# Optimization experiments

Measured on AMD Instinct MI355X. Metric: run time of the kernel, lower is better.

The kernel has to match this reference:

```python
import jax, jax.numpy as jnp
import numpy as np
from jax import lax


def setup_inputs() -> dict:
    key = jax.random.key(0)
    k1, k2 = jax.random.split(key)
    B, N, C, H, W = 4, 32, 32, 64, 64
    x = jax.random.normal(k1, (B, N, C, H, W), dtype=jnp.float32)
    # grouped conv weight: groups = N*C, 1 input channel per group, 3 outputs per group
    w = jax.random.normal(k2, (3 * N * C, 1, 1, 1), dtype=jnp.float32) * 0.1
    return {"x": x, "w": w}


def reference(x, w):
    B, N, C, H, W = x.shape
    xc = x.reshape(B, N * C, H, W)
    # grouped 1x1 conv (groups = N*C), matches nn.Conv2d(inC*N, 3*qkvC*N, 1, groups=qkvC*N, bias=False)
    qkv = lax.conv_general_dilated(
        xc, w,
        window_strides=(1, 1), padding=[(0, 0), (0, 0)],
        feature_group_count=N * C,
        dimension_numbers=("NCHW", "OIHW", "NCHW"),
    )
    qkv = qkv.reshape(B, N, C, 3, H, W)
    scale = (H * W) ** (-0.5)
    q = scale * qkv[:, :, :, 0]           # (B,N,C,H,W)
    k = qkv[:, :, :, 1]
    v = qkv[:, :, :, 2]
    # original: 6D einsum (a,b,c,d,e,f) then sum over d,e == contraction over H,W
    S = jnp.einsum("bachw,bfchw->bcaf", q, k)   # (B,C,N,N)
    A = jax.nn.softmax(S, axis=-1)
    # original: broadcast-multiply with v and sum over f
    out = jnp.einsum("bcaf,bfchw->abchw", A, v)  # (N,B,C,H,W)
    return out
```

## Files before the change

### kernel.cpp

```cpp
#include <hip/hip_runtime.h>

typedef __attribute__((ext_vector_type(8))) short bf16x8;
typedef __attribute__((ext_vector_type(4))) float f32x4;

#define BB 4
#define NN 32
#define CC 32
#define HWD 4096
#define AROW ((size_t)CC * HWD)

__device__ __forceinline__ unsigned cvt_pk_bf16(float lo, float hi) {
    unsigned r;
    asm("v_cvt_pk_bf16_f32 %0, %1, %2" : "=v"(r) : "v"(lo), "v"(hi));
    return r;
}

__device__ __forceinline__ bf16x8 pack8(float4 a, float4 b) {
    union { unsigned u[4]; bf16x8 v; } u;
    u.u[0] = cvt_pk_bf16(a.x, a.y);
    u.u[1] = cvt_pk_bf16(a.z, a.w);
    u.u[2] = cvt_pk_bf16(b.x, b.y);
    u.u[3] = cvt_pk_bf16(b.z, b.w);
    return u.v;
}

__global__ __launch_bounds__(256) void k_gram(const float* __restrict__ x,
                                              float* __restrict__ Gp) {
    const int bid = blockIdx.x;
    const int s   = bid & 7;
    const int bc  = bid >> 3;
    const int b   = bc >> 5, c = bc & 31;
    const int tid = threadIdx.x;
    const int w   = tid >> 6, l = tid & 63;
    const int r   = l & 15, g = l >> 4;

    const float* xb = x + ((size_t)b * NN * CC + c) * HWD;
    const int hwbase = s * 512 + w * 128;
    const float* p0 = xb + (size_t)r        * AROW + hwbase + 8 * g;
    const float* p1 = xb + (size_t)(r + 16) * AROW + hwbase + 8 * g;

    f32x4 acc[2][2];
#pragma unroll
    for (int i = 0; i < 2; ++i)
#pragma unroll
        for (int j = 0; j < 2; ++j)
#pragma unroll
            for (int q = 0; q < 4; ++q) acc[i][j][q] = 0.f;

#pragma unroll
    for (int ch = 0; ch < 4; ++ch) {
        const float4 a0 = *(const float4*)(p0 + ch * 32);
        const float4 a1 = *(const float4*)(p0 + ch * 32 + 4);
        const float4 b0 = *(const float4*)(p1 + ch * 32);
        const float4 b1 = *(const float4*)(p1 + ch * 32 + 4);
        const bf16x8 F0 = pack8(a0, a1);
        const bf16x8 F1 = pack8(b0, b1);
        acc[0][0] = __builtin_amdgcn_mfma_f32_16x16x32_bf16(F0, F0, acc[0][0], 0, 0, 0);
        acc[0][1] = __builtin_amdgcn_mfma_f32_16x16x32_bf16(F0, F1, acc[0][1], 0, 0, 0);
        acc[1][0] = __builtin_amdgcn_mfma_f32_16x16x32_bf16(F1, F0, acc[1][0], 0, 0, 0);
        acc[1][1] = __builtin_amdgcn_mfma_f32_16x16x32_bf16(F1, F1, acc[1][1], 0, 0, 0);
    }

    __shared__ float red[4][64][16];
#pragma unroll
    for (int ta = 0; ta < 2; ++ta)
#pragma unroll
        for (int tf = 0; tf < 2; ++tf)
#pragma unroll
            for (int q = 0; q < 4; ++q)
                red[w][l][(ta * 2 + tf) * 4 + q] = acc[ta][tf][q];
    __syncthreads();

    const int a   = tid >> 3;
    const int f0  = 4 * (tid & 7);
    const int lg  = ((a >> 2) & 3) * 16 + (f0 & 15);
    const int reg = ((a >> 4) * 2 + (f0 >> 4)) * 4 + (a & 3);
    float sv[4];
#pragma unroll
    for (int j = 0; j < 4; ++j) {
        float v = 0.f;
#pragma unroll
        for (int ww = 0; ww < 4; ++ww) v += red[ww][lg + j][reg];
        sv[j] = v;
    }
    *(float4*)&Gp[(size_t)bid * 1024 + 4 * tid] = make_float4(sv[0], sv[1], sv[2], sv[3]);
}

__global__ __launch_bounds__(256) void k_pv(const float* __restrict__ x,
                                            const float* __restrict__ w,
                                            const float* __restrict__ Gp,
                                            float* __restrict__ out) {
    const int bid   = blockIdx.x;
    const int chunk = bid & 15;
    const int bc    = bid >> 4;
    const int b     = bc >> 5, c = bc & 31;
    const int tid   = threadIdx.x;
    const int wv    = tid >> 6, l = tid & 63;
    const int r     = l & 15, g = l >> 4;

    __shared__ unsigned xt[256][16];
    __shared__ unsigned ahat[32][20];

    {
        const int a = tid >> 3, fo = 4 * (tid & 7);
        float gs[4] = {0.f, 0.f, 0.f, 0.f};
#pragma unroll
        for (int s = 0; s < 8; ++s) {
            const float4 v = *(const float4*)&Gp[(size_t)(bc * 8 + s) * 1024 + a * 32 + fo];
            gs[0] += v.x; gs[1] += v.y; gs[2] += v.z; gs[3] += v.w;
        }
        const float wq = w[(a * CC + c) * 3] * 0.015625f;
        float S[4];
#pragma unroll
        for (int j = 0; j < 4; ++j)
            S[j] = wq * w[((fo + j) * CC + c) * 3 + 1] * gs[j];

        float m = fmaxf(fmaxf(S[0], S[1]), fmaxf(S[2], S[3]));
#pragma unroll
        for (int o = 1; o < 8; o <<= 1) m = fmaxf(m, __shfl_xor(m, o, 64));
        float e[4], sum = 0.f;
#pragma unroll
        for (int j = 0; j < 4; ++j) { e[j] = __expf(S[j] - m); sum += e[j]; }
#pragma unroll
        for (int o = 1; o < 8; o <<= 1) sum += __shfl_xor(sum, o, 64);
        const float inv = 1.f / sum;

        const float o0 = e[0] * inv * w[((fo + 0) * CC + c) * 3 + 2];
        const float o1 = e[1] * inv * w[((fo + 1) * CC + c) * 3 + 2];
        const float o2 = e[2] * inv * w[((fo + 2) * CC + c) * 3 + 2];
        const float o3 = e[3] * inv * w[((fo + 3) * CC + c) * 3 + 2];
        ahat[a][2 * (tid & 7) + 0] = cvt_pk_bf16(o0, o1);
        ahat[a][2 * (tid & 7) + 1] = cvt_pk_bf16(o2, o3);
    }

    {
        const int p = tid >> 4;
        const int q = tid & 15;
        const float* xr0 = x + ((size_t)(b * NN + 2 * p) * CC + c) * HWD + chunk * 256;
        const float* xr1 = xr0 + AROW;
#pragma unroll
        for (int k = 0; k < 4; ++k) {
            const int hwc = 4 * (q + 16 * k);
            const float4 fa = *(const float4*)(xr0 + hwc);
            const float4 fb = *(const float4*)(xr1 + hwc);
            const float av[4] = {fa.x, fa.y, fa.z, fa.w};
            const float bv[4] = {fb.x, fb.y, fb.z, fb.w};
#pragma unroll
            for (int i = 0; i < 4; ++i) {
                const int hw = hwc + i;
                xt[hw][p ^ (hw & 12)] = cvt_pk_bf16(av[i], bv[i]);
            }
        }
    }
    __syncthreads();

    const bf16x8 A0 = *(const bf16x8*)&ahat[r][4 * g];
    const bf16x8 A1 = *(const bf16x8*)&ahat[r + 16][4 * g];
    const f32x4 zero = {0.f, 0.f, 0.f, 0.f};

#pragma unroll
    for (int ht = 0; ht < 4; ++ht) {
        const int hw = wv * 64 + ht * 16 + r;
        const bf16x8 B = *(const bf16x8*)&xt[hw][4 * (g ^ ((hw >> 2) & 3))];
        f32x4 d0 = __builtin_amdgcn_mfma_f32_16x16x32_bf16(A0, B, zero, 0, 0, 0);
        f32x4 d1 = __builtin_amdgcn_mfma_f32_16x16x32_bf16(A1, B, zero, 0, 0, 0);

        const size_t hwg = (size_t)chunk * 256 + hw;
#pragma unroll
        for (int q2 = 0; q2 < 4; ++q2) {
            const int a0r = g * 4 + q2;
            out[(((size_t)a0r * BB + b) * CC + c) * HWD + hwg]        = d0[q2];
            out[(((size_t)(a0r + 16) * BB + b) * CC + c) * HWD + hwg] = d1[q2];
        }
    }
}

extern "C" void kernel_launch(void* const* d_in, const int* in_sizes, int n_in,
                              void* d_out, int out_size, void* d_ws, size_t ws_size,
                              hipStream_t stream) {
    const float* x = (const float*)d_in[0];
    const float* w = (const float*)d_in[1];
    float* outp = (float*)d_out;
    float* Gp = (float*)d_ws;

    hipLaunchKernelGGL(k_gram, dim3(1024), dim3(256), 0, stream, x, Gp);
    hipLaunchKernelGGL(k_pv,   dim3(2048), dim3(256), 0, stream, x, w, Gp, outp);
}
```

Before: 45.81 us.

## Fuse gram and PV kernels into one launch with last-block softmax and flag spin-wait

Merges the two kernels into a single 1024-block kernel. Each block computes its partial Gram slice, and the last block per (b,c), found via an atomic counter, reduces the slices, applies the softmax and writes the bf16 A-hat to global memory. It then releases a flag that the other blocks spin on before each does two PV chunks. This removes one kernel launch and the serialization gap between them, and lets blocks reuse x while it is likely still cached. In exchange it adds a memset, spin-waits that rely on all blocks of a group being co-resident, and atomic-load overhead.

```diff
diff --git a/kernel.cpp b/kernel.cpp
--- a/kernel.cpp
+++ b/kernel.cpp
@@ -8,6 +8,10 @@
 #define CC 32
 #define HWD 4096
 #define AROW ((size_t)CC * HWD)
+
+#define GP_BYTES   ((size_t)4 * 1024 * 1024)
+#define AHAT_BYTES ((size_t)256 * 1024)
+#define CTRL_OFF   (GP_BYTES + AHAT_BYTES)
 
 __device__ __forceinline__ unsigned cvt_pk_bf16(float lo, float hi) {
     unsigned r;
@@ -24,90 +28,97 @@
     return u.v;
 }
 
-__global__ __launch_bounds__(256) void k_gram(const float* __restrict__ x,
-                                              float* __restrict__ Gp) {
+__global__ __launch_bounds__(256, 4) void k_all(const float* __restrict__ x,
+                                                const float* __restrict__ w,
+                                                float* __restrict__ Gp,
+                                                unsigned* __restrict__ Ahat,
+                                                unsigned* __restrict__ cnt,
+                                                unsigned* __restrict__ flag,
+                                                float* __restrict__ out) {
     const int bid = blockIdx.x;
     const int s   = bid & 7;
     const int bc  = bid >> 3;
     const int b   = bc >> 5, c = bc & 31;
     const int tid = threadIdx.x;
-    const int w   = tid >> 6, l = tid & 63;
+    const int wv  = tid >> 6, l = tid & 63;
     const int r   = l & 15, g = l >> 4;
 
-    const float* xb = x + ((size_t)b * NN * CC + c) * HWD;
-    const int hwbase = s * 512 + w * 128;
-    const float* p0 = xb + (size_t)r        * AROW + hwbase + 8 * g;
-    const float* p1 = xb + (size_t)(r + 16) * AROW + hwbase + 8 * g;
-
-    f32x4 acc[2][2];
-#pragma unroll
-    for (int i = 0; i < 2; ++i)
-#pragma unroll
-        for (int j = 0; j < 2; ++j)
-#pragma unroll
-            for (int q = 0; q < 4; ++q) acc[i][j][q] = 0.f;
-
-#pragma unroll
-    for (int ch = 0; ch < 4; ++ch) {
-        const float4 a0 = *(const float4*)(p0 + ch * 32);
-        const float4 a1 = *(const float4*)(p0 + ch * 32 + 4);
-        const float4 b0 = *(const float4*)(p1 + ch * 32);
-        const float4 b1 = *(const float4*)(p1 + ch * 32 + 4);
-        const bf16x8 F0 = pack8(a0, a1);
-        const bf16x8 F1 = pack8(b0, b1);
-        acc[0][0] = __builtin_amdgcn_mfma_f32_16x16x32_bf16(F0, F0, acc[0][0], 0, 0, 0);
-        acc[0][1] = __builtin_amdgcn_mfma_f32_16x16x32_bf16(F0, F1, acc[0][1], 0, 0, 0);
-        acc[1][0] = __builtin_amdgcn_mfma_f32_16x16x32_bf16(F1, F0, acc[1][0], 0, 0, 0);
-        acc[1][1] = __builtin_amdgcn_mfma_f32_16x16x32_bf16(F1, F1, acc[1][1], 0, 0, 0);
-    }
-
-    __shared__ float red[4][64][16];
-#pragma unroll
-    for (int ta = 0; ta < 2; ++ta)
-#pragma unroll
-        for (int tf = 0; tf < 2; ++tf)
-#pragma unroll
-            for (int q = 0; q < 4; ++q)
-                red[w][l][(ta * 2 + tf) * 4 + q] = acc[ta][tf][q];
+    __shared__ union {
+        float red[4][64][16];
+        unsigned xt[256][16];
+    } sm;
+    __shared__ unsigned is_last;
+
+    {
+        const float* xb = x + ((size_t)b * NN * CC + c) * HWD;
+        const int hwbase = s * 512 + wv * 128;
+        const float* p0 = xb + (size_t)r        * AROW + hwbase + 8 * g;
+        const float* p1 = xb + (size_t)(r + 16) * AROW + hwbase + 8 * g;
+
+        f32x4 acc[2][2];
+#pragma unroll
+        for (int i = 0; i < 2; ++i)
+#pragma unroll
+            for (int j = 0; j < 2; ++j)
+#pragma unroll
+                for (int q = 0; q < 4; ++q) acc[i][j][q] = 0.f;
+
+#pragma unroll
+        for (int ch = 0; ch < 4; ++ch) {
+            const float4 a0 = *(const float4*)(p0 + ch * 32);
+            const float4 a1 = *(const float4*)(p0 + ch * 32 + 4);
+            const float4 b0 = *(const float4*)(p1 + ch * 32);
+            const float4 b1 = *(const float4*)(p1 + ch * 32 + 4);
+            const bf16x8 F0 = pack8(a0, a1);
+            const bf16x8 F1 = pack8(b0, b1);
+            acc[0][0] = __builtin_amdgcn_mfma_f32_16x16x32_bf16(F0, F0, acc[0][0], 0, 0, 0);
+            acc[0][1] = __builtin_amdgcn_mfma_f32_16x16x32_bf16(F0, F1, acc[0][1], 0, 0, 0);
+            acc[1][0] = __builtin_amdgcn_mfma_f32_16x16x32_bf16(F1, F0, acc[1][0], 0, 0, 0);
+            acc[1][1] = __builtin_amdgcn_mfma_f32_16x16x32_bf16(F1, F1, acc[1][1], 0, 0, 0);
+        }
+
+#pragma unroll
+        for (int ta = 0; ta < 2; ++ta)
+#pragma unroll
+            for (int tf = 0; tf < 2; ++tf)
+#pragma unroll
+                for (int q = 0; q < 4; ++q)
+                    sm.red[wv][l][(ta * 2 + tf) * 4 + q] = acc[ta][tf][q];
+        __syncthreads();
+
+        const int a   = tid >> 3;
+        const int f0  = 4 * (tid & 7);
+        const int lg  = ((a >> 2) & 3) * 16 + (f0 & 15);
+        const int reg = ((a >> 4) * 2 + (f0 >> 4)) * 4 + (a & 3);
+        float sv[4];
+#pragma unroll
+        for (int j = 0; j < 4; ++j) {
+            float v = 0.f;
+#pragma unroll
+            for (int ww = 0; ww < 4; ++ww) v += sm.red[ww][lg + j][reg];
+            sv[j] = v;
+        }
+        *(float4*)&Gp[(size_t)bid * 1024 + 4 * tid] = make_float4(sv[0], sv[1], sv[2], sv[3]);
+    }
+
     __syncthreads();
-
-    const int a   = tid >> 3;
-    const int f0  = 4 * (tid & 7);
-    const int lg  = ((a >> 2) & 3) * 16 + (f0 & 15);
-    const int reg = ((a >> 4) * 2 + (f0 >> 4)) * 4 + (a & 3);
-    float sv[4];
-#pragma unroll
-    for (int j = 0; j < 4; ++j) {
-        float v = 0.f;
-#pragma unroll
-        for (int ww = 0; ww < 4; ++ww) v += red[ww][lg + j][reg];
-        sv[j] = v;
-    }
-    *(float4*)&Gp[(size_t)bid * 1024 + 4 * tid] = make_float4(sv[0], sv[1], sv[2], sv[3]);
-}
-
-__global__ __launch_bounds__(256) void k_pv(const float* __restrict__ x,
-                                            const float* __restrict__ w,
-                                            const float* __restrict__ Gp,
-                                            float* __restrict__ out) {
-    const int bid   = blockIdx.x;
-    const int chunk = bid & 15;
-    const int bc    = bid >> 4;
-    const int b     = bc >> 5, c = bc & 31;
-    const int tid   = threadIdx.x;
-    const int wv    = tid >> 6, l = tid & 63;
-    const int r     = l & 15, g = l >> 4;
-
-    __shared__ unsigned xt[256][16];
-    __shared__ unsigned ahat[32][20];
-
-    {
+    if (tid == 0) {
+        __threadfence();
+        unsigned old = atomicAdd(&cnt[bc], 1u);
+        is_last = (old == 7u) ? 1u : 0u;
+    }
+    __syncthreads();
+
+    if (is_last) {
         const int a = tid >> 3, fo = 4 * (tid & 7);
         float gs[4] = {0.f, 0.f, 0.f, 0.f};
 #pragma unroll
-        for (int s = 0; s < 8; ++s) {
-            const float4 v = *(const float4*)&Gp[(size_t)(bc * 8 + s) * 1024 + a * 32 + fo];
-            gs[0] += v.x; gs[1] += v.y; gs[2] += v.z; gs[3] += v.w;
+        for (int s2 = 0; s2 < 8; ++s2) {
+            const float* gp = &Gp[(size_t)(bc * 8 + s2) * 1024 + a * 32 + fo];
+            gs[0] += __hip_atomic_load(gp + 0, __ATOMIC_RELAXED, __HIP_MEMORY_SCOPE_AGENT);
+            gs[1] += __hip_atomic_load(gp + 1, __ATOMIC_RELAXED, __HIP_MEMORY_SCOPE_AGENT);
+            gs[2] += __hip_atomic_load(gp + 2, __ATOMIC_RELAXED, __HIP_MEMORY_SCOPE_AGENT);
+            gs[3] += __hip_atomic_load(gp + 3, __ATOMIC_RELAXED, __HIP_MEMORY_SCOPE_AGENT);
         }
         const float wq = w[(a * CC + c) * 3] * 0.015625f;
         float S[4];
@@ -129,48 +140,75 @@
         const float o1 = e[1] * inv * w[((fo + 1) * CC + c) * 3 + 2];
         const float o2 = e[2] * inv * w[((fo + 2) * CC + c) * 3 + 2];
         const float o3 = e[3] * inv * w[((fo + 3) * CC + c) * 3 + 2];
-        ahat[a][2 * (tid & 7) + 0] = cvt_pk_bf16(o0, o1);
-        ahat[a][2 * (tid & 7) + 1] = cvt_pk_bf16(o2, o3);
-    }
-
+        unsigned* ad = Ahat + (size_t)bc * 512 + a * 16 + 2 * (tid & 7);
+        __hip_atomic_store(ad + 0, cvt_pk_bf16(o0, o1), __ATOMIC_RELAXED, __HIP_MEMORY_SCOPE_AGENT);
+        __hip_atomic_store(ad + 1, cvt_pk_bf16(o2, o3), __ATOMIC_RELAXED, __HIP_MEMORY_SCOPE_AGENT);
+        __syncthreads();
+        if (tid == 0) {
+            __threadfence();
+            __hip_atomic_store(&flag[bc], 1u, __ATOMIC_RELEASE, __HIP_MEMORY_SCOPE_AGENT);
+        }
+    }
+
+    if (tid == 0) {
+        while (__hip_atomic_load(&flag[bc], __ATOMIC_ACQUIRE, __HIP_MEMORY_SCOPE_AGENT) == 0u)
+            __builtin_amdgcn_s_sleep(2);
+    }
+    __syncthreads();
+
+    union { unsigned u[4]; bf16x8 v; } ua0, ua1;
     {
-        const int p = tid >> 4;
-        const int q = tid & 15;
-        const float* xr0 = x + ((size_t)(b * NN + 2 * p) * CC + c) * HWD + chunk * 256;
-        const float* xr1 = xr0 + AROW;
-#pragma unroll
-        for (int k = 0; k < 4; ++k) {
-            const int hwc = 4 * (q + 16 * k);
-            const float4 fa = *(const float4*)(xr0 + hwc);
-            const float4 fb = *(const float4*)(xr1 + hwc);
-            const float av[4] = {fa.x, fa.y, fa.z, fa.w};
-            const float bv[4] = {fb.x, fb.y, fb.z, fb.w};
-#pragma unroll
-            for (int i = 0; i < 4; ++i) {
-                const int hw = hwc + i;
-                xt[hw][p ^ (hw & 12)] = cvt_pk_bf16(av[i], bv[i]);
+        const unsigned* ad = Ahat + (size_t)bc * 512;
+#pragma unroll
+        for (int i = 0; i < 4; ++i) {
+            ua0.u[i] = __hip_atomic_load(ad + r * 16 + 4 * g + i,
+                                         __ATOMIC_RELAXED, __HIP_MEMORY_SCOPE_AGENT);
+            ua1.u[i] = __hip_atomic_load(ad + (r + 16) * 16 + 4 * g + i,
+                                         __ATOMIC_RELAXED, __HIP_MEMORY_SCOPE_AGENT);
+        }
+    }
+
+    const f32x4 zero = {0.f, 0.f, 0.f, 0.f};
+#pragma clang loop unroll(disable)
+    for (int ck = 0; ck < 2; ++ck) {
+        const int chunk = 2 * s + ck;
+        __syncthreads();
+
+        {
+            const int p = tid >> 4;
+            const int q = tid & 15;
+            const float* xr0 = x + ((size_t)(b * NN + 2 * p) * CC + c) * HWD + chunk * 256;
+            const float* xr1 = xr0 + AROW;
+#pragma unroll
+            for (int k = 0; k < 4; ++k) {
+                const int hwc = 4 * (q + 16 * k);
+                const float4 fa = *(const float4*)(xr0 + hwc);
+                const float4 fb = *(const float4*)(xr1 + hwc);
+                const float av[4] = {fa.x, fa.y, fa.z, fa.w};
+                const float bv[4] = {fb.x, fb.y, fb.z, fb.w};
+#pragma unroll
+                for (int i = 0; i < 4; ++i) {
+                    const int hw = hwc + i;
+                    sm.xt[hw][p ^ (hw & 12)] = cvt_pk_bf16(av[i], bv[i]);
+                }
             }
         }
-    }
-    __syncthreads();
-
-    const bf16x8 A0 = *(const bf16x8*)&ahat[r][4 * g];
-    const bf16x8 A1 = *(const bf16x8*)&ahat[r + 16][4 * g];
-    const f32x4 zero = {0.f, 0.f, 0.f, 0.f};
-
-#pragma unroll
-    for (int ht = 0; ht < 4; ++ht) {
-        const int hw = wv * 64 + ht * 16 + r;
-        const bf16x8 B = *(const bf16x8*)&xt[hw][4 * (g ^ ((hw >> 2) & 3))];
-        f32x4 d0 = __builtin_amdgcn_mfma_f32_16x16x32_bf16(A0, B, zero, 0, 0, 0);
-        f32x4 d1 = __builtin_amdgcn_mfma_f32_16x16x32_bf16(A1, B, zero, 0, 0, 0);
-
-        const size_t hwg = (size_t)chunk * 256 + hw;
-#pragma unroll
-        for (int q2 = 0; q2 < 4; ++q2) {
-            const int a0r = g * 4 + q2;
-            out[(((size_t)a0r * BB + b) * CC + c) * HWD + hwg]        = d0[q2];
-            out[(((size_t)(a0r + 16) * BB + b) * CC + c) * HWD + hwg] = d1[q2];
+        __syncthreads();
+
+#pragma unroll
+        for (int ht = 0; ht < 4; ++ht) {
+            const int hw = wv * 64 + ht * 16 + r;
+            const bf16x8 B = *(const bf16x8*)&sm.xt[hw][4 * (g ^ ((hw >> 2) & 3))];
+            f32x4 d0 = __builtin_amdgcn_mfma_f32_16x16x32_bf16(ua0.v, B, zero, 0, 0, 0);
+            f32x4 d1 = __builtin_amdgcn_mfma_f32_16x16x32_bf16(ua1.v, B, zero, 0, 0, 0);
+
+            const size_t hwg = (size_t)chunk * 256 + hw;
+#pragma unroll
+            for (int q2 = 0; q2 < 4; ++q2) {
+                const int a0r = g * 4 + q2;
+                out[(((size_t)a0r * BB + b) * CC + c) * HWD + hwg]        = d0[q2];
+                out[(((size_t)(a0r + 16) * BB + b) * CC + c) * HWD + hwg] = d1[q2];
+            }
         }
     }
 }
@@ -181,8 +219,13 @@
     const float* x = (const float*)d_in[0];
     const float* w = (const float*)d_in[1];
     float* outp = (float*)d_out;
-    float* Gp = (float*)d_ws;
-
-    hipLaunchKernelGGL(k_gram, dim3(1024), dim3(256), 0, stream, x, Gp);
-    hipLaunchKernelGGL(k_pv,   dim3(2048), dim3(256), 0, stream, x, w, Gp, outp);
-}
+    float* Gp      = (float*)d_ws;
+    unsigned* Ahat = (unsigned*)((char*)d_ws + GP_BYTES);
+    unsigned* ctrl = (unsigned*)((char*)d_ws + CTRL_OFF);
+    unsigned* cnt  = ctrl;
+    unsigned* flag = ctrl + 128;
+
+    hipMemsetAsync((void*)ctrl, 0, 1024, stream);
+    hipLaunchKernelGGL(k_all, dim3(1024), dim3(256), 0, stream,
+                       x, w, Gp, Ahat, cnt, flag, outp);
+}
```

Result: slower. 147.2 us (+221.3%).
